# Optimization experiments

Hardware: AMD Instinct MI355X
Metric: run time of the kernel (lower is better)

## Reference

```python
import jax, jax.numpy as jnp
import numpy as np
from jax import lax

DIM = 256
HEADS = 8
C3 = DIM * 3 // 4  # 192
C1 = DIM // 4      # 64


def conv1x1(x, w):
    # x: [b,c,h,w], w: [o,c] (1x1 conv, no bias)
    return jnp.einsum('bchw,oc->bohw', x, w)


def dwconv3x3(x, w):
    # x: [b,c,h,w], w: [c,1,3,3] depthwise
    return lax.conv_general_dilated(
        x, w, window_strides=(1, 1), padding='SAME',
        feature_group_count=x.shape[1],
        dimension_numbers=('NCHW', 'OIHW', 'NCHW'))


def l2norm(x, eps=1e-12):
    # torch F.normalize: x / max(||x||, eps) along last dim
    n = jnp.sqrt(jnp.sum(x * x, axis=-1, keepdims=True))
    return x / jnp.maximum(n, eps)


def setup_inputs() -> dict:
    key = jax.random.key(0)
    ks = jax.random.split(key, 10)
    s = 0.02
    return {
        'x': jax.random.normal(ks[0], (4, DIM, 128, 128), jnp.float32),
        'k_v': jax.random.normal(ks[1], (4, 256), jnp.float32),
        'temperature': jnp.ones((HEADS, 1, 1), jnp.float32),
        'w_kR': jax.random.normal(ks[2], (C3, 192), jnp.float32) * s,
        'w_kI': jax.random.normal(ks[3], (C1, 64), jnp.float32) * s,
        'w_qR': jax.random.normal(ks[4], (DIM, C3), jnp.float32) * s,
        'w_qdw': jax.random.normal(ks[5], (DIM, 1, 3, 3), jnp.float32) * s,
        'w_kvI': jax.random.normal(ks[6], (2 * DIM, C1), jnp.float32) * s,
        'w_kvdw': jax.random.normal(ks[7], (2 * DIM, 1, 3, 3), jnp.float32) * s,
        'w_proj': jax.random.normal(ks[8], (DIM, DIM), jnp.float32) * s,
    }


def reference(x, k_v, temperature, w_kR, w_kI, w_qR, w_qdw, w_kvI, w_kvdw, w_proj):
    b, c, h, w = x.shape
    # FiLM-style modulation: x * kv + x
    kvr = (k_v[:, :192] @ w_kR.T)[:, :, None, None]  # [b, C3, 1, 1]
    kvi = (k_v[:, 192:] @ w_kI.T)[:, :, None, None]  # [b, C1, 1, 1]
    x_r = x[:, :C3] * kvr + x[:, :C3]
    x_i = x[:, C3:] * kvi + x[:, C3:]
    # QKV projections
    q = dwconv3x3(conv1x1(x_r, w_qR), w_qdw)          # [b, dim, h, w]
    kv = dwconv3x3(conv1x1(x_i, w_kvI), w_kvdw)       # [b, 2*dim, h, w]
    k, v = jnp.split(kv, 2, axis=1)
    hd = DIM // HEADS
    hw = h * w
    q = q.reshape(b, HEADS, hd, hw)
    k = k.reshape(b, HEADS, hd, hw)
    v = v.reshape(b, HEADS, hd, hw)
    # channel-wise (transposed) attention with L2 norm + temperature
    q = l2norm(q)
    k = l2norm(k)
    attn = jnp.einsum('bhcn,bhdn->bhcd', q, k) * temperature  # [b,H,hd,hd]
    attn = jax.nn.softmax(attn, axis=-1)
    out = jnp.einsum('bhcd,bhdn->bhcn', attn, v)
    out = out.reshape(b, DIM, h, w)
    return conv1x1(out, w_proj)
```

## Files before the change

kernel.cpp:

```cpp
#include <hip/hip_runtime.h>
#include <math.h>

#define HW 16384

typedef unsigned int uint;
typedef short bfrag __attribute__((ext_vector_type(8)));
typedef float f32x4 __attribute__((ext_vector_type(4)));

union FragCvt { uint4 u; bfrag v; };

__device__ inline uint pack2bf(float a, float b) {
  uint ua = __builtin_bit_cast(uint, a);
  uint ub = __builtin_bit_cast(uint, b);
  ua = (ua + 0x7FFFu + ((ua >> 16) & 1u)) >> 16;
  ub = (ub + 0x7FFFu + ((ub >> 16) & 1u)) & 0xFFFF0000u;
  return ua | ub;
}

__global__ __launch_bounds__(256) void mod_kernel(
    const float* __restrict__ kv, const float* __restrict__ wkR,
    const float* __restrict__ wkI, float* __restrict__ mod)
{
  int b = blockIdx.x;
  int c = threadIdx.x;
  const float* kvb = kv + b * 256;
  float s = 0.f;
  if (c < 192) {
    const float* wr = wkR + c * 192;
    for (int j = 0; j < 192; ++j) s += kvb[j] * wr[j];
  } else {
    const float* wi = wkI + (c - 192) * 64;
    for (int j = 0; j < 64; ++j) s += kvb[192 + j] * wi[j];
  }
  mod[b * 256 + c] = 1.f + s;
}

__global__ __launch_bounds__(256) void mgemm(
    const float* __restrict__ W, int ldW, size_t Wbstride,
    const float* __restrict__ X, int c0, size_t Xbstride,
    const float* __restrict__ mod,
    float* __restrict__ Y, size_t Ybstride, int K)
{
  int b = blockIdx.z, mt = blockIdx.y, nt = blockIdx.x;
  const float* Wb = W + (size_t)b * Wbstride + (size_t)mt * 128 * ldW;
  const float* Xb = X + (size_t)b * Xbstride + (size_t)c0 * HW + nt * 128;
  float* Yb = Y + (size_t)b * Ybstride + (size_t)mt * 128 * HW + nt * 128;

  __shared__ unsigned short Al[128 * 40];
  __shared__ unsigned short Bl[128 * 40];

  int t = threadIdx.x;
  int w = t >> 6, l = t & 63;
  int wm = (w >> 1) * 64, wn = (w & 1) * 64;
  int lm = l & 15, lk = (l >> 4) * 8;

  int am = t >> 1, ako = (t & 1) * 16;
  int bn = t & 127, bo = (t >> 7) * 8;

  f32x4 acc[4][4];
  #pragma unroll
  for (int fi = 0; fi < 4; ++fi)
    #pragma unroll
    for (int fj = 0; fj < 4; ++fj) acc[fi][fj] = {0.f, 0.f, 0.f, 0.f};

  for (int k0 = 0; k0 < K; k0 += 32) {
    const float* wsrc = Wb + (size_t)am * ldW + k0 + ako;
    float4 a0 = *(const float4*)(wsrc);
    float4 a1 = *(const float4*)(wsrc + 4);
    float4 a2 = *(const float4*)(wsrc + 8);
    float4 a3 = *(const float4*)(wsrc + 12);

    float xr[2][8];
    #pragma unroll
    for (int i = 0; i < 2; ++i) {
      int kb = k0 + bo + i * 16;
      #pragma unroll
      for (int r = 0; r < 8; ++r)
        xr[i][r] = Xb[(size_t)(kb + r) * HW + bn];
    }
    float sc[2][8];
    if (mod) {
      const float* mp = mod + b * 256 + c0 + k0 + bo;
      #pragma unroll
      for (int i = 0; i < 2; ++i) {
        float4 m0 = *(const float4*)(mp + i * 16);
        float4 m1 = *(const float4*)(mp + i * 16 + 4);
        sc[i][0] = m0.x; sc[i][1] = m0.y; sc[i][2] = m0.z; sc[i][3] = m0.w;
        sc[i][4] = m1.x; sc[i][5] = m1.y; sc[i][6] = m1.z; sc[i][7] = m1.w;
      }
    } else {
      #pragma unroll
      for (int i = 0; i < 2; ++i)
        #pragma unroll
        for (int r = 0; r < 8; ++r) sc[i][r] = 1.f;
    }

    __syncthreads();

    uint4 aw0, aw1;
    aw0.x = pack2bf(a0.x, a0.y); aw0.y = pack2bf(a0.z, a0.w);
    aw0.z = pack2bf(a1.x, a1.y); aw0.w = pack2bf(a1.z, a1.w);
    aw1.x = pack2bf(a2.x, a2.y); aw1.y = pack2bf(a2.z, a2.w);
    aw1.z = pack2bf(a3.x, a3.y); aw1.w = pack2bf(a3.z, a3.w);
    *(uint4*)&Al[am * 40 + ako] = aw0;
    *(uint4*)&Al[am * 40 + ako + 8] = aw1;

    #pragma unroll
    for (int i = 0; i < 2; ++i) {
      uint4 bw;
      bw.x = pack2bf(xr[i][0] * sc[i][0], xr[i][1] * sc[i][1]);
      bw.y = pack2bf(xr[i][2] * sc[i][2], xr[i][3] * sc[i][3]);
      bw.z = pack2bf(xr[i][4] * sc[i][4], xr[i][5] * sc[i][5]);
      bw.w = pack2bf(xr[i][6] * sc[i][6], xr[i][7] * sc[i][7]);
      *(uint4*)&Bl[bn * 40 + bo + i * 16] = bw;
    }

    __syncthreads();

    bfrag af[4], bfr[4];
    #pragma unroll
    for (int fi = 0; fi < 4; ++fi) {
      FragCvt cv;
      cv.u = *(const uint4*)&Al[(wm + fi * 16 + lm) * 40 + lk];
      af[fi] = cv.v;
    }
    #pragma unroll
    for (int fj = 0; fj < 4; ++fj) {
      FragCvt cv;
      cv.u = *(const uint4*)&Bl[(wn + fj * 16 + lm) * 40 + lk];
      bfr[fj] = cv.v;
    }
    #pragma unroll
    for (int fi = 0; fi < 4; ++fi)
      #pragma unroll
      for (int fj = 0; fj < 4; ++fj)
        acc[fi][fj] = __builtin_amdgcn_mfma_f32_16x16x32_bf16(
            af[fi], bfr[fj], acc[fi][fj], 0, 0, 0);
  }

  int orow = (l >> 4) * 4;
  #pragma unroll
  for (int fi = 0; fi < 4; ++fi)
    #pragma unroll
    for (int fj = 0; fj < 4; ++fj)
      #pragma unroll
      for (int r = 0; r < 4; ++r)
        Yb[(size_t)(wm + fi * 16 + orow + r) * HW + (wn + fj * 16 + lm)] =
            acc[fi][fj][r];
}

__global__ __launch_bounds__(256) void dwconv_kernel(
    const float* __restrict__ in, size_t in_bstride,
    const float* __restrict__ wdw,
    float* __restrict__ out, size_t out_bstride,
    float* __restrict__ ssq)
{
  int c = blockIdx.x;
  int b = blockIdx.y;
  int t = threadIdx.x;
  int r = t >> 5;
  int xq = t & 31;

  const float4* ip4 = (const float4*)(in + (size_t)b * in_bstride + ((size_t)c << 14));
  float4* op4 = (float4*)(out + (size_t)b * out_bstride + ((size_t)c << 14));
  const float* wp = wdw + c * 9;
  float w0 = wp[0], w1 = wp[1], w2 = wp[2], w3 = wp[3], w4 = wp[4],
        w5 = wp[5], w6 = wp[6], w7 = wp[7], w8 = wp[8];

  const float4 z4 = make_float4(0.f, 0.f, 0.f, 0.f);
  int y0 = r << 4;

  float4 a = (y0 > 0) ? ip4[((y0 - 1) << 5) + xq] : z4;
  float4 bb = ip4[(y0 << 5) + xq];

  float aL = __shfl_up(a.w, 1);  if (xq == 0)  aL = 0.f;
  float aR = __shfl_down(a.x, 1); if (xq == 31) aR = 0.f;
  float bL = __shfl_up(bb.w, 1); if (xq == 0)  bL = 0.f;
  float bR = __shfl_down(bb.x, 1); if (xq == 31) bR = 0.f;

  float ss = 0.f;
  #pragma unroll
  for (int i = 0; i < 16; ++i) {
    int y = y0 + i;
    int yc = (y + 1 < 128) ? (y + 1) : 127;
    float4 cc = ip4[(yc << 5) + xq];
    if (y + 1 >= 128) { cc.x = 0.f; cc.y = 0.f; cc.z = 0.f; cc.w = 0.f; }
    float cL = __shfl_up(cc.w, 1);  if (xq == 0)  cL = 0.f;
    float cR = __shfl_down(cc.x, 1); if (xq == 31) cR = 0.f;

    float4 o;
    o.x = w0 * aL  + w1 * a.x + w2 * a.y +
          w3 * bL  + w4 * bb.x + w5 * bb.y +
          w6 * cL  + w7 * cc.x + w8 * cc.y;
    o.y = w0 * a.x + w1 * a.y + w2 * a.z +
          w3 * bb.x + w4 * bb.y + w5 * bb.z +
          w6 * cc.x + w7 * cc.y + w8 * cc.z;
    o.z = w0 * a.y + w1 * a.z + w2 * a.w +
          w3 * bb.y + w4 * bb.z + w5 * bb.w +
          w6 * cc.y + w7 * cc.z + w8 * cc.w;
    o.w = w0 * a.z + w1 * a.w + w2 * aR +
          w3 * bb.z + w4 * bb.w + w5 * bR +
          w6 * cc.z + w7 * cc.w + w8 * cR;

    op4[(y << 5) + xq] = o;
    ss += o.x * o.x + o.y * o.y + o.z * o.z + o.w * o.w;

    a = bb; aL = bL; aR = bR;
    bb = cc; bL = cL; bR = cR;
  }

  if (ssq) {
    #pragma unroll
    for (int off = 32; off > 0; off >>= 1) ss += __shfl_down(ss, off);
    __shared__ float red[4];
    if ((t & 63) == 0) red[t >> 6] = ss;
    __syncthreads();
    if (t == 0) ssq[b * 256 + c] = red[0] + red[1] + red[2] + red[3];
  }
}

__global__ __launch_bounds__(256) void gram_kernel(
    const float* __restrict__ qdw, const float* __restrict__ kdw,
    float* __restrict__ S)
{
  int chunk = blockIdx.x, h = blockIdx.y, b = blockIdx.z;
  __shared__ float Qs[32][68];
  __shared__ float Ks[32][68];
  int t = threadIdx.x;
  int wave = t >> 6, lane = t & 63;
  int c0 = lane >> 3, d0 = lane & 7;
  float acc[4][4];
  #pragma unroll
  for (int i = 0; i < 4; ++i)
    #pragma unroll
    for (int j = 0; j < 4; ++j) acc[i][j] = 0.f;

  const float* qb = qdw + (((size_t)b * 256 + h * 32) << 14) + chunk * 1024;
  const float* kb = kdw + (((size_t)b * 256 + h * 32) << 14) + chunk * 1024;
  int lch = t >> 4;
  int lpx = (t & 15) << 2;

  for (int sub = 0; sub < 16; ++sub) {
    float4 qa = *(const float4*)(qb + ((size_t)lch << 14) + sub * 64 + lpx);
    float4 qc = *(const float4*)(qb + ((size_t)(lch + 16) << 14) + sub * 64 + lpx);
    float4 ka = *(const float4*)(kb + ((size_t)lch << 14) + sub * 64 + lpx);
    float4 kc = *(const float4*)(kb + ((size_t)(lch + 16) << 14) + sub * 64 + lpx);
    __syncthreads();
    *(float4*)&Qs[lch][lpx] = qa;
    *(float4*)&Qs[lch + 16][lpx] = qc;
    *(float4*)&Ks[lch][lpx] = ka;
    *(float4*)&Ks[lch + 16][lpx] = kc;
    __syncthreads();
    #pragma unroll
    for (int pg = 0; pg < 4; ++pg) {
      int p0 = (wave << 4) + (pg << 2);
      float4 q0 = *(float4*)&Qs[c0][p0];
      float4 q1 = *(float4*)&Qs[c0 + 8][p0];
      float4 q2 = *(float4*)&Qs[c0 + 16][p0];
      float4 q3 = *(float4*)&Qs[c0 + 24][p0];
      float4 k0v = *(float4*)&Ks[d0][p0];
      float4 k1v = *(float4*)&Ks[d0 + 8][p0];
      float4 k2v = *(float4*)&Ks[d0 + 16][p0];
      float4 k3v = *(float4*)&Ks[d0 + 24][p0];
      float qv[4][4] = {{q0.x, q0.y, q0.z, q0.w}, {q1.x, q1.y, q1.z, q1.w},
                        {q2.x, q2.y, q2.z, q2.w}, {q3.x, q3.y, q3.z, q3.w}};
      float kv[4][4] = {{k0v.x, k0v.y, k0v.z, k0v.w}, {k1v.x, k1v.y, k1v.z, k1v.w},
                        {k2v.x, k2v.y, k2v.z, k2v.w}, {k3v.x, k3v.y, k3v.z, k3v.w}};
      #pragma unroll
      for (int i = 0; i < 4; ++i)
        #pragma unroll
        for (int j = 0; j < 4; ++j)
          acc[i][j] += qv[i][0] * kv[j][0] + qv[i][1] * kv[j][1] +
                       qv[i][2] * kv[j][2] + qv[i][3] * kv[j][3];
    }
  }
  float* Sp = S + (((size_t)b * 8 + h) << 10);
  #pragma unroll
  for (int i = 0; i < 4; ++i)
    #pragma unroll
    for (int j = 0; j < 4; ++j)
      atomicAdd(&Sp[(c0 + 8 * i) * 32 + d0 + 8 * j], acc[i][j]);
}

__global__ __launch_bounds__(64) void softmax_kernel(
    float* __restrict__ S, const float* __restrict__ ssq,
    const float* __restrict__ ssk, const float* __restrict__ temp)
{
  int bh = blockIdx.x;
  int b = bh >> 3, h = bh & 7;
  int c = threadIdx.x;
  if (c >= 32) return;
  float* row = S + ((size_t)bh << 10) + c * 32;
  float invq = 1.f / fmaxf(sqrtf(ssq[b * 256 + h * 32 + c]), 1e-12f);
  float T = temp[h];
  float lg[32];
  float mx = -1e30f;
  for (int d = 0; d < 32; ++d) {
    float invk = 1.f / fmaxf(sqrtf(ssk[b * 256 + h * 32 + d]), 1e-12f);
    float v = row[d] * invq * invk * T;
    lg[d] = v;
    mx = fmaxf(mx, v);
  }
  float sum = 0.f;
  for (int d = 0; d < 32; ++d) { float e = expf(lg[d] - mx); lg[d] = e; sum += e; }
  float inv = 1.f / sum;
  for (int d = 0; d < 32; ++d) row[d] = lg[d] * inv;
}

__global__ __launch_bounds__(256) void mbuild_kernel(
    const float* __restrict__ attn, const float* __restrict__ wproj,
    float* __restrict__ M)
{
  int o = blockIdx.x, b = blockIdx.y;
  int col = threadIdx.x;
  int h = col >> 5, d = col & 31;
  const float* a = attn + (((size_t)b * 8 + h) << 10);
  const float* wp = wproj + o * 256 + h * 32;
  float s = 0.f;
  #pragma unroll
  for (int cc = 0; cc < 32; ++cc) s += wp[cc] * a[cc * 32 + d];
  M[((size_t)b * 256 + o) * 256 + col] = s;
}

extern "C" void kernel_launch(void* const* d_in, const int* in_sizes, int n_in,
                              void* d_out, int out_size, void* d_ws, size_t ws_size,
                              hipStream_t stream)
{
  const float* x      = (const float*)d_in[0];
  const float* k_v    = (const float*)d_in[1];
  const float* temp   = (const float*)d_in[2];
  const float* w_kR   = (const float*)d_in[3];
  const float* w_kI   = (const float*)d_in[4];
  const float* w_qR   = (const float*)d_in[5];
  const float* w_qdw  = (const float*)d_in[6];
  const float* w_kvI  = (const float*)d_in[7];
  const float* w_kvdw = (const float*)d_in[8];
  const float* w_proj = (const float*)d_in[9];
  float* out = (float*)d_out;

  float* ws   = (float*)d_ws;
  float* bufA = ws;
  float* bufB = ws + 16777216;
  float* bufC = ws + 33554432;
  float* sm   = ws + 50331648;
  float* mod  = sm;
  float* ssq  = sm + 1024;
  float* ssk  = sm + 2048;
  float* S    = sm + 3072;
  float* M    = sm + 3072 + 32768;

  hipMemsetAsync(S, 0, (size_t)32768 * sizeof(float), stream);

  mod_kernel<<<dim3(4), dim3(256), 0, stream>>>(k_v, w_kR, w_kI, mod);

  mgemm<<<dim3(128, 2, 4), dim3(256), 0, stream>>>(
      w_kvI, 64, 0, x, 192, 4194304, mod, bufA, 4194304, 64);
  dwconv_kernel<<<dim3(256, 4), dim3(256), 0, stream>>>(
      bufA, 4194304, w_kvdw, bufB, 4194304, ssk);

  mgemm<<<dim3(128, 2, 4), dim3(256), 0, stream>>>(
      w_qR, 192, 0, x, 0, 4194304, mod, bufA, 4194304, 192);
  dwconv_kernel<<<dim3(256, 4), dim3(256), 0, stream>>>(
      bufA, 4194304, w_qdw, bufC, 4194304, ssq);

  gram_kernel<<<dim3(16, 8, 4), dim3(256), 0, stream>>>(bufC, bufB, S);

  mgemm<<<dim3(128, 2, 4), dim3(256), 0, stream>>>(
      w_kvI + 256 * 64, 64, 0, x, 192, 4194304, mod, bufA, 4194304, 64);

  softmax_kernel<<<dim3(32), dim3(64), 0, stream>>>(S, ssq, ssk, temp);
  mbuild_kernel<<<dim3(256, 4), dim3(256), 0, stream>>>(S, w_proj, M);

  dwconv_kernel<<<dim3(256, 4), dim3(256), 0, stream>>>(
      bufA, 4194304, w_kvdw + 256 * 9, bufC, 4194304, (float*)nullptr);

  mgemm<<<dim3(128, 2, 4), dim3(256), 0, stream>>>(
      M, 256, 65536, bufC, 0, 4194304, (const float*)nullptr, out, 4194304, 256);
}
```

Before: 335.4 us.

## Fuse Q/K depthwise convs and sum-of-squares into the Gram kernel

The two depthwise 3x3 convs for Q and K, with their per-channel sum-of-squares, are folded into the Gram-matrix kernel. Each block convolves 8 image rows of its head's Q and K channels straight into shared memory and then accumulates QK^T from there. This removes two kernel launches and the full-size write and re-read of the convolved Q and K tensors. In exchange, rows above and below each tile are loaded redundantly, the norms are accumulated with atomics into a now-zeroed buffer, and register pressure per thread is higher.

```diff
diff --git a/kernel.cpp b/kernel.cpp
--- a/kernel.cpp
+++ b/kernel.cpp
@@ -152,8 +152,7 @@
 __global__ __launch_bounds__(256) void dwconv_kernel(
     const float* __restrict__ in, size_t in_bstride,
     const float* __restrict__ wdw,
-    float* __restrict__ out, size_t out_bstride,
-    float* __restrict__ ssq)
+    float* __restrict__ out, size_t out_bstride)
 {
   int c = blockIdx.x;
   int b = blockIdx.y;
@@ -178,7 +177,6 @@
   float bL = __shfl_up(bb.w, 1); if (xq == 0)  bL = 0.f;
   float bR = __shfl_down(bb.x, 1); if (xq == 31) bR = 0.f;
 
-  float ss = 0.f;
   #pragma unroll
   for (int i = 0; i < 16; ++i) {
     int y = y0 + i;
@@ -203,77 +201,129 @@
           w6 * cc.z + w7 * cc.w + w8 * cR;
 
     op4[(y << 5) + xq] = o;
-    ss += o.x * o.x + o.y * o.y + o.z * o.z + o.w * o.w;
 
     a = bb; aL = bL; aR = bR;
     bb = cc; bL = cL; bR = cR;
   }
-
-  if (ssq) {
-    #pragma unroll
-    for (int off = 32; off > 0; off >>= 1) ss += __shfl_down(ss, off);
-    __shared__ float red[4];
-    if ((t & 63) == 0) red[t >> 6] = ss;
-    __syncthreads();
-    if (t == 0) ssq[b * 256 + c] = red[0] + red[1] + red[2] + red[3];
-  }
-}
-
-__global__ __launch_bounds__(256) void gram_kernel(
-    const float* __restrict__ qdw, const float* __restrict__ kdw,
+}
+
+__global__ __launch_bounds__(256, 2) void dwgram_kernel(
+    const float* __restrict__ qpre, const float* __restrict__ kpre,
+    const float* __restrict__ wqdw, const float* __restrict__ wkdw,
+    float* __restrict__ ssq, float* __restrict__ ssk,
     float* __restrict__ S)
 {
-  int chunk = blockIdx.x, h = blockIdx.y, b = blockIdx.z;
-  __shared__ float Qs[32][68];
-  __shared__ float Ks[32][68];
+  int chunk = blockIdx.x;
+  int h = blockIdx.y, b = blockIdx.z;
   int t = threadIdx.x;
+  int ch = t >> 2;
+  int xq = t & 3;
+  int cl = ch & 31;
+  bool isq = ch < 32;
+
+  __shared__ float Qs[32][132];
+  __shared__ float Ks[32][132];
+
+  const float* src = (isq ? qpre : kpre) +
+      (size_t)b * 4194304 + ((size_t)(h * 32 + cl) << 14) + (xq << 5);
+  const float* wp = (isq ? wqdw : wkdw) + (h * 32 + cl) * 9;
+  float w0 = wp[0], w1 = wp[1], w2 = wp[2], w3 = wp[3], w4 = wp[4],
+        w5 = wp[5], w6 = wp[6], w7 = wp[7], w8 = wp[8];
+
   int wave = t >> 6, lane = t & 63;
   int c0 = lane >> 3, d0 = lane & 7;
+  int p0 = wave << 5;
+
   float acc[4][4];
   #pragma unroll
   for (int i = 0; i < 4; ++i)
     #pragma unroll
     for (int j = 0; j < 4; ++j) acc[i][j] = 0.f;
-
-  const float* qb = qdw + (((size_t)b * 256 + h * 32) << 14) + chunk * 1024;
-  const float* kb = kdw + (((size_t)b * 256 + h * 32) << 14) + chunk * 1024;
-  int lch = t >> 4;
-  int lpx = (t & 15) << 2;
-
-  for (int sub = 0; sub < 16; ++sub) {
-    float4 qa = *(const float4*)(qb + ((size_t)lch << 14) + sub * 64 + lpx);
-    float4 qc = *(const float4*)(qb + ((size_t)(lch + 16) << 14) + sub * 64 + lpx);
-    float4 ka = *(const float4*)(kb + ((size_t)lch << 14) + sub * 64 + lpx);
-    float4 kc = *(const float4*)(kb + ((size_t)(lch + 16) << 14) + sub * 64 + lpx);
+  float ss = 0.f;
+
+  const float4 z4 = make_float4(0.f, 0.f, 0.f, 0.f);
+  int y0 = chunk * 8;
+  float* drow = (isq ? &Qs[cl][0] : &Ks[cl][0]) + (xq << 5);
+
+  for (int i = 0; i < 8; ++i) {
+    int y = y0 + i;
+    bool hm = (y > 0), hp = (y < 127);
+    const float* rm = src + ((y - 1) << 7);
+    const float* r0 = src + (y << 7);
+    const float* rp = src + ((y + 1) << 7);
+
+    float4 ra[8], rb[8], rc[8];
+    #pragma unroll
+    for (int g = 0; g < 8; ++g) {
+      ra[g] = hm ? *(const float4*)(rm + 4 * g) : z4;
+      rb[g] = *(const float4*)(r0 + 4 * g);
+      rc[g] = hp ? *(const float4*)(rp + 4 * g) : z4;
+    }
+    float haL = __shfl_up(ra[7].w, 1);  if (xq == 0) haL = 0.f;
+    float haR = __shfl_down(ra[0].x, 1); if (xq == 3) haR = 0.f;
+    float hbL = __shfl_up(rb[7].w, 1);  if (xq == 0) hbL = 0.f;
+    float hbR = __shfl_down(rb[0].x, 1); if (xq == 3) hbR = 0.f;
+    float hcL = __shfl_up(rc[7].w, 1);  if (xq == 0) hcL = 0.f;
+    float hcR = __shfl_down(rc[0].x, 1); if (xq == 3) hcR = 0.f;
+
     __syncthreads();
-    *(float4*)&Qs[lch][lpx] = qa;
-    *(float4*)&Qs[lch + 16][lpx] = qc;
-    *(float4*)&Ks[lch][lpx] = ka;
-    *(float4*)&Ks[lch + 16][lpx] = kc;
+
+    #pragma unroll
+    for (int g = 0; g < 8; ++g) {
+      float aL = (g == 0) ? haL : ra[g - 1].w;
+      float aR = (g == 7) ? haR : ra[g + 1].x;
+      float bL = (g == 0) ? hbL : rb[g - 1].w;
+      float bR = (g == 7) ? hbR : rb[g + 1].x;
+      float cL = (g == 0) ? hcL : rc[g - 1].w;
+      float cR = (g == 7) ? hcR : rc[g + 1].x;
+      float4 o;
+      o.x = w0 * aL      + w1 * ra[g].x + w2 * ra[g].y +
+            w3 * bL      + w4 * rb[g].x + w5 * rb[g].y +
+            w6 * cL      + w7 * rc[g].x + w8 * rc[g].y;
+      o.y = w0 * ra[g].x + w1 * ra[g].y + w2 * ra[g].z +
+            w3 * rb[g].x + w4 * rb[g].y + w5 * rb[g].z +
+            w6 * rc[g].x + w7 * rc[g].y + w8 * rc[g].z;
+      o.z = w0 * ra[g].y + w1 * ra[g].z + w2 * ra[g].w +
+            w3 * rb[g].y + w4 * rb[g].z + w5 * rb[g].w +
+            w6 * rc[g].y + w7 * rc[g].z + w8 * rc[g].w;
+      o.w = w0 * ra[g].z + w1 * ra[g].w + w2 * aR +
+            w3 * rb[g].z + w4 * rb[g].w + w5 * bR +
+            w6 * rc[g].z + w7 * rc[g].w + w8 * cR;
+      *(float4*)(drow + 4 * g) = o;
+      ss += o.x * o.x + o.y * o.y + o.z * o.z + o.w * o.w;
+    }
+
     __syncthreads();
-    #pragma unroll
-    for (int pg = 0; pg < 4; ++pg) {
-      int p0 = (wave << 4) + (pg << 2);
-      float4 q0 = *(float4*)&Qs[c0][p0];
-      float4 q1 = *(float4*)&Qs[c0 + 8][p0];
-      float4 q2 = *(float4*)&Qs[c0 + 16][p0];
-      float4 q3 = *(float4*)&Qs[c0 + 24][p0];
-      float4 k0v = *(float4*)&Ks[d0][p0];
-      float4 k1v = *(float4*)&Ks[d0 + 8][p0];
-      float4 k2v = *(float4*)&Ks[d0 + 16][p0];
-      float4 k3v = *(float4*)&Ks[d0 + 24][p0];
+
+    #pragma unroll
+    for (int pg = 0; pg < 8; ++pg) {
+      int p = p0 + (pg << 2);
+      float4 q0 = *(float4*)&Qs[c0][p];
+      float4 q1 = *(float4*)&Qs[c0 + 8][p];
+      float4 q2 = *(float4*)&Qs[c0 + 16][p];
+      float4 q3 = *(float4*)&Qs[c0 + 24][p];
+      float4 k0 = *(float4*)&Ks[d0][p];
+      float4 k1 = *(float4*)&Ks[d0 + 8][p];
+      float4 k2 = *(float4*)&Ks[d0 + 16][p];
+      float4 k3 = *(float4*)&Ks[d0 + 24][p];
       float qv[4][4] = {{q0.x, q0.y, q0.z, q0.w}, {q1.x, q1.y, q1.z, q1.w},
                         {q2.x, q2.y, q2.z, q2.w}, {q3.x, q3.y, q3.z, q3.w}};
-      float kv[4][4] = {{k0v.x, k0v.y, k0v.z, k0v.w}, {k1v.x, k1v.y, k1v.z, k1v.w},
-                        {k2v.x, k2v.y, k2v.z, k2v.w}, {k3v.x, k3v.y, k3v.z, k3v.w}};
-      #pragma unroll
-      for (int i = 0; i < 4; ++i)
+      float kv[4][4] = {{k0.x, k0.y, k0.z, k0.w}, {k1.x, k1.y, k1.z, k1.w},
+                        {k2.x, k2.y, k2.z, k2.w}, {k3.x, k3.y, k3.z, k3.w}};
+      #pragma unroll
+      for (int ii = 0; ii < 4; ++ii)
         #pragma unroll
-        for (int j = 0; j < 4; ++j)
-          acc[i][j] += qv[i][0] * kv[j][0] + qv[i][1] * kv[j][1] +
-                       qv[i][2] * kv[j][2] + qv[i][3] * kv[j][3];
+        for (int jj = 0; jj < 4; ++jj)
+          acc[ii][jj] += qv[ii][0] * kv[jj][0] + qv[ii][1] * kv[jj][1] +
+                         qv[ii][2] * kv[jj][2] + qv[ii][3] * kv[jj][3];
     }
   }
+
+  ss += __shfl_xor(ss, 1);
+  ss += __shfl_xor(ss, 2);
+  if (xq == 0)
+    atomicAdd((isq ? ssq : ssk) + b * 256 + h * 32 + cl, ss);
+
   float* Sp = S + (((size_t)b * 8 + h) << 10);
   #pragma unroll
   for (int i = 0; i < 4; ++i)
@@ -349,31 +399,27 @@
   float* S    = sm + 3072;
   float* M    = sm + 3072 + 32768;
 
-  hipMemsetAsync(S, 0, (size_t)32768 * sizeof(float), stream);
+  hipMemsetAsync(ssq, 0, (size_t)(1024 + 1024 + 32768) * sizeof(float), stream);
 
   mod_kernel<<<dim3(4), dim3(256), 0, stream>>>(k_v, w_kR, w_kI, mod);
 
   mgemm<<<dim3(128, 2, 4), dim3(256), 0, stream>>>(
       w_kvI, 64, 0, x, 192, 4194304, mod, bufA, 4194304, 64);
-  dwconv_kernel<<<dim3(256, 4), dim3(256), 0, stream>>>(
-      bufA, 4194304, w_kvdw, bufB, 4194304, ssk);
-
   mgemm<<<dim3(128, 2, 4), dim3(256), 0, stream>>>(
-      w_qR, 192, 0, x, 0, 4194304, mod, bufA, 4194304, 192);
-  dwconv_kernel<<<dim3(256, 4), dim3(256), 0, stream>>>(
-      bufA, 4194304, w_qdw, bufC, 4194304, ssq);
-
-  gram_kernel<<<dim3(16, 8, 4), dim3(256), 0, stream>>>(bufC, bufB, S);
+      w_qR, 192, 0, x, 0, 4194304, mod, bufB, 4194304, 192);
+
+  dwgram_kernel<<<dim3(16, 8, 4), dim3(256), 0, stream>>>(
+      bufB, bufA, w_qdw, w_kvdw, ssq, ssk, S);
 
   mgemm<<<dim3(128, 2, 4), dim3(256), 0, stream>>>(
-      w_kvI + 256 * 64, 64, 0, x, 192, 4194304, mod, bufA, 4194304, 64);
+      w_kvI + 256 * 64, 64, 0, x, 192, 4194304, mod, bufC, 4194304, 64);
 
   softmax_kernel<<<dim3(32), dim3(64), 0, stream>>>(S, ssq, ssk, temp);
   mbuild_kernel<<<dim3(256, 4), dim3(256), 0, stream>>>(S, w_proj, M);
 
   dwconv_kernel<<<dim3(256, 4), dim3(256), 0, stream>>>(
-      bufA, 4194304, w_kvdw + 256 * 9, bufC, 4194304, (float*)nullptr);
+      bufC, 4194304, w_kvdw + 256 * 9, bufB, 4194304);
 
   mgemm<<<dim3(128, 2, 4), dim3(256), 0, stream>>>(
-      M, 256, 65536, bufC, 0, 4194304, (const float*)nullptr, out, 4194304, 256);
-}
+      M, 256, 65536, bufB, 0, 4194304, (const float*)nullptr, out, 4194304, 256);
+}
```

New measurement: 600.5 us. 1.79x slower.
